# Performance work log

Measured on AMD Instinct MI355X. Metric: run time of the kernel, lower is better.

Reference implementation:

```python
import jax, jax.numpy as jnp
import numpy as np

B, T, C = 4, 2048, 1024
H = 16
D = C // H  # head_dim = 64


def setup_inputs() -> dict:
    key = jax.random.key(0)
    k1, k2, k3 = jax.random.split(key, 3)
    scale = 0.02
    x = jax.random.normal(k1, (B, T, C), dtype=jnp.float32)
    w_attn = jax.random.normal(k2, (C, 3 * C), dtype=jnp.float32) * scale
    b_attn = jnp.zeros((3 * C,), dtype=jnp.float32)
    w_proj = jax.random.normal(k3, (C, C), dtype=jnp.float32) * scale
    b_proj = jnp.zeros((C,), dtype=jnp.float32)
    return {"x": x, "w_attn": w_attn, "b_attn": b_attn,
            "w_proj": w_proj, "b_proj": b_proj}


def reference(x, w_attn, b_attn, w_proj, b_proj):
    Bc, Tc, Cc = x.shape
    qkv = x @ w_attn + b_attn                      # [B, T, 3C]
    q, k, v = jnp.split(qkv, 3, axis=-1)
    # [B, H, T, D]
    q = q.reshape(Bc, Tc, H, D).transpose(0, 2, 1, 3)
    k = k.reshape(Bc, Tc, H, D).transpose(0, 2, 1, 3)
    v = v.reshape(Bc, Tc, H, D).transpose(0, 2, 1, 3)
    att = jnp.einsum('bhqd,bhkd->bhqk', q, k) / jnp.sqrt(jnp.float32(D))
    causal = jnp.tril(jnp.ones((Tc, Tc), dtype=bool))
    att = jnp.where(causal, att, -jnp.inf)
    att = jax.nn.softmax(att, axis=-1)
    y = jnp.einsum('bhqk,bhkd->bhqd', att, v)      # [B, H, T, D]
    y = y.transpose(0, 2, 1, 3).reshape(Bc, Tc, Cc)
    return y @ w_proj + b_proj
```

## Files before the change

kernel.cpp:

```cpp
#include <hip/hip_runtime.h>

typedef unsigned short u16;
typedef __bf16 bf16x8 __attribute__((ext_vector_type(8)));
typedef float f32x4 __attribute__((ext_vector_type(4)));

#define T_SEQ 2048
#define NH 16
#define HD 64
#define CDIM 1024

__device__ __forceinline__ u16 f2bf(float f) {
    union { float f; unsigned int u; } v; v.f = f;
    unsigned int r = v.u + 0x7FFFu + ((v.u >> 16) & 1u);
    return (u16)(r >> 16);
}

__device__ __forceinline__ unsigned cvt_pk_bf16(float lo, float hi) {
    unsigned r;
    asm("v_cvt_pk_bf16_f32 %0, %1, %2" : "=v"(r) : "v"(lo), "v"(hi));
    return r;
}

__device__ __forceinline__ void gll16(const u16* g, const u16* l) {
    __builtin_amdgcn_global_load_lds((const __attribute__((address_space(1))) void*)g,
                                     (__attribute__((address_space(3))) void*)l, 16, 0, 0);
}

__global__ void cast_f32_bf16(const float* __restrict__ in, u16* __restrict__ out, int n) {
    int i = (blockIdx.x * blockDim.x + threadIdx.x) * 4;
    if (i >= n) return;
    float4 v = *reinterpret_cast<const float4*>(in + i);
    ushort4 o;
    o.x = f2bf(v.x); o.y = f2bf(v.y); o.z = f2bf(v.z); o.w = f2bf(v.w);
    *reinterpret_cast<ushort4*>(out + i) = o;
}

__global__ void transpose_cast(const float* __restrict__ in, u16* __restrict__ out, int K, int N) {
    __shared__ float tile[32][33];
    int n0 = blockIdx.x * 32, k0 = blockIdx.y * 32;
    int tx = threadIdx.x & 31, ty = threadIdx.x >> 5;
#pragma unroll
    for (int i = 0; i < 32; i += 8)
        tile[ty + i][tx] = in[(size_t)(k0 + ty + i) * N + n0 + tx];
    __syncthreads();
#pragma unroll
    for (int i = 0; i < 32; i += 8)
        out[(size_t)(n0 + ty + i) * K + k0 + tx] = f2bf(tile[tx][ty + i]);
}

__global__ void vtrans(const u16* __restrict__ in, u16* __restrict__ out) {
    __shared__ u16 tl[32][34];
    int x0 = blockIdx.x * 32;
    int y0 = blockIdx.y * 32;
    int z = blockIdx.z;
    int tx = threadIdx.x & 31, ty = threadIdx.x >> 5;
    const size_t ib = (size_t)z * T_SEQ * HD;
    const size_t ob = (size_t)z * HD * T_SEQ;
#pragma unroll
    for (int i = 0; i < 32; i += 8)
        tl[ty + i][tx] = in[ib + (size_t)(x0 + ty + i) * HD + y0 + tx];
    __syncthreads();
#pragma unroll
    for (int i = 0; i < 32; i += 8)
        out[ob + (size_t)(y0 + ty + i) * T_SEQ + x0 + tx] = tl[tx][ty + i];
}

template <int EPI>
__global__ __launch_bounds__(256)
void gemm_bt(const u16* __restrict__ A, const u16* __restrict__ Bt,
             const float* __restrict__ bias, float* __restrict__ out,
             u16* __restrict__ qb, u16* __restrict__ kb, u16* __restrict__ vb,
             int M, int N, int K) {
    __shared__ u16 As[128 * 64];
    __shared__ u16 Bs[128 * 64];
    const int tid = threadIdx.x;
    const int lane = tid & 63;
    const int w = tid >> 6;
    const int wm = w >> 1, wn = w & 1;
    const int c = lane & 15, g = lane >> 4;
    const int gm0 = blockIdx.y * 128;
    const int gn0 = blockIdx.x * 128;

    f32x4 acc[4][4] = {};

    for (int k0 = 0; k0 < K; k0 += 64) {
#pragma unroll
        for (int it = 0; it < 4; ++it) {
            int tb = it * 256 + w * 64;
            int task = tb + lane;
            int r = task >> 3, sl = task & 7;
            int sc = sl ^ (r & 7);
            gll16(A + (size_t)(gm0 + r) * K + k0 + sc * 8, As + (size_t)task * 8);
            gll16(Bt + (size_t)(gn0 + r) * K + k0 + sc * 8, Bs + (size_t)task * 8);
        }
        __syncthreads();
#pragma unroll
        for (int kk = 0; kk < 2; ++kk) {
            bf16x8 a[4], b[4];
#pragma unroll
            for (int m = 0; m < 4; ++m) {
                int row = wm * 64 + m * 16 + c;
                a[m] = *reinterpret_cast<const bf16x8*>(&As[row * 64 + (((kk * 4 + g) ^ (c & 7)) * 8)]);
            }
#pragma unroll
            for (int n = 0; n < 4; ++n) {
                int row = wn * 64 + n * 16 + c;
                b[n] = *reinterpret_cast<const bf16x8*>(&Bs[row * 64 + (((kk * 4 + g) ^ (c & 7)) * 8)]);
            }
#pragma unroll
            for (int m = 0; m < 4; ++m)
#pragma unroll
                for (int n = 0; n < 4; ++n)
                    acc[m][n] = __builtin_amdgcn_mfma_f32_16x16x32_bf16(a[m], b[n], acc[m][n], 0, 0, 0);
        }
        __syncthreads();
    }

#pragma unroll
    for (int m = 0; m < 4; ++m) {
#pragma unroll
        for (int n = 0; n < 4; ++n) {
            int gcol = gn0 + wn * 64 + n * 16 + c;
            float bv = bias[gcol];
#pragma unroll
            for (int r = 0; r < 4; ++r) {
                int grow = gm0 + wm * 64 + m * 16 + g * 4 + r;
                float v = acc[m][n][r] + bv;
                if (EPI == 1) {
                    out[(size_t)grow * N + gcol] = v;
                } else {
                    int which = gcol >> 10;
                    int cc = gcol & 1023;
                    int h = cc >> 6, d = cc & 63;
                    int b_ = grow >> 11, t = grow & 2047;
                    int bh = b_ * NH + h;
                    u16 bvv = (which == 0) ? f2bf(v * 0.18033688f) : f2bf(v);
                    u16* dst = (which == 0) ? qb : (which == 1) ? kb : vb;
                    dst[((size_t)bh * T_SEQ + t) * HD + d] = bvv;
                }
            }
        }
    }
}

__global__ __launch_bounds__(512, 4)
void attn_fwd(const u16* __restrict__ Qb, const u16* __restrict__ Kb,
              const u16* __restrict__ Vt, u16* __restrict__ yb) {
    __shared__ u16 Ks[2][64 * 64];
    __shared__ u16 Vs[2][64 * 64];
    __shared__ unsigned Ps[8][1024];
    const int tid = threadIdx.x, lane = tid & 63, w = tid >> 6;
    const int g = lane >> 4, c = lane & 15;
    const int f = blockIdx.x;
    const int xcd = f & 7, j = (f >> 3) & 7, bhi = f >> 6;
    const int bh = xcd * 8 + bhi;
    const int b = bh >> 4, hh = bh & 15;
    const float NEG = -1e30f;
    const size_t kBase = (size_t)bh * T_SEQ * HD;
    const size_t vBase = (size_t)bh * HD * T_SEQ;
    unsigned* ps = &Ps[w][0];
    const int sw = c & 7;
    const int qwv[2] = {(15 - j) * 128 + w * 16, j * 128 + w * 16};

    bf16x8 qf[2][2];
#pragma unroll
    for (int u = 0; u < 2; ++u) {
        const u16* qrow = Qb + kBase + (size_t)(qwv[u] + c) * HD;
        qf[u][0] = *reinterpret_cast<const bf16x8*>(qrow + g * 8);
        qf[u][1] = *reinterpret_cast<const bf16x8*>(qrow + 32 + g * 8);
    }

    f32x4 yacc[2][4] = {};
    float l[2] = {0.f, 0.f};
    const int nt = 2 * (15 - j) + 2;
    int cur = 0;

    {
        int r = tid >> 3, sl = tid & 7, sc = sl ^ (r & 7);
        gll16(Kb + kBase + (size_t)r * HD + sc * 8, Ks[0] + (size_t)tid * 8);
        gll16(Vt + vBase + (size_t)r * T_SEQ + sc * 8, Vs[0] + (size_t)tid * 8);
        __syncthreads();
    }

    for (int kt = 0; kt < nt; ++kt) {
        const int kv0 = kt * 64;
        const bool more = (kt + 1 < nt);
        if (more) {
            const int nv0 = kv0 + 64;
            int r = tid >> 3, sl = tid & 7, sc = sl ^ (r & 7);
            gll16(Kb + kBase + (size_t)(nv0 + r) * HD + sc * 8, Ks[cur ^ 1] + (size_t)tid * 8);
            gll16(Vt + vBase + (size_t)r * T_SEQ + nv0 + sc * 8, Vs[cur ^ 1] + (size_t)tid * 8);
        }
        const u16* ks = Ks[cur];
        const u16* vs = Vs[cur];
        const bool a0 = (kv0 <= qwv[0] + 15);
        const bool a1 = (kv0 <= qwv[1] + 15);

        if (a0 || a1) {
            f32x4 s_[2][4];
            __builtin_amdgcn_s_setprio(1);
#pragma unroll
            for (int n = 0; n < 4; ++n) {
                int rb = (n * 16 + c) * 64;
                bf16x8 k0 = *reinterpret_cast<const bf16x8*>(&ks[rb + ((g ^ sw) * 8)]);
                bf16x8 k1 = *reinterpret_cast<const bf16x8*>(&ks[rb + (((4 + g) ^ sw) * 8)]);
                if (a0) {
                    f32x4 t = {};
                    t = __builtin_amdgcn_mfma_f32_16x16x32_bf16(k0, qf[0][0], t, 0, 0, 0);
                    t = __builtin_amdgcn_mfma_f32_16x16x32_bf16(k1, qf[0][1], t, 0, 0, 0);
                    s_[0][n] = t;
                }
                if (a1) {
                    f32x4 t = {};
                    t = __builtin_amdgcn_mfma_f32_16x16x32_bf16(k0, qf[1][0], t, 0, 0, 0);
                    t = __builtin_amdgcn_mfma_f32_16x16x32_bf16(k1, qf[1][1], t, 0, 0, 0);
                    s_[1][n] = t;
                }
            }
            __builtin_amdgcn_s_setprio(0);

            bf16x8 pa[2][2];
#pragma unroll
            for (int u = 0; u < 2; ++u) {
                const bool act = u ? a1 : a0;
                if (act) {
                    const int qwu = qwv[u];
                    if (kv0 + 63 > qwu) {
                        int q = qwu + c;
#pragma unroll
                        for (int n = 0; n < 4; ++n) {
                            int kvb = kv0 + n * 16 + 4 * g;
#pragma unroll
                            for (int r = 0; r < 4; ++r)
                                if (kvb + r > q) s_[u][n][r] = NEG;
                        }
                    }
                    float rsum = 0.f;
                    int base = (16 * u + c) * 32;
#pragma unroll
                    for (int n = 0; n < 4; ++n) {
                        float p0 = __builtin_amdgcn_exp2f(s_[u][n][0]);
                        float p1 = __builtin_amdgcn_exp2f(s_[u][n][1]);
                        float p2 = __builtin_amdgcn_exp2f(s_[u][n][2]);
                        float p3 = __builtin_amdgcn_exp2f(s_[u][n][3]);
                        rsum += (p0 + p1) + (p2 + p3);
                        uint2 pr;
                        pr.x = cvt_pk_bf16(p0, p1);
                        pr.y = cvt_pk_bf16(p2, p3);
                        *reinterpret_cast<uint2*>(&ps[base + ((n ^ (c & 3)) << 3) + 2 * g]) = pr;
                    }
                    l[u] += rsum;
#pragma unroll
                    for (int kk = 0; kk < 2; ++kk) {
                        int idx = (16 * u + c) * 32 + ((kk * 16 + 4 * g) ^ ((c & 3) << 3));
                        pa[u][kk] = *reinterpret_cast<const bf16x8*>(&ps[idx]);
                    }
                }
            }
            __builtin_amdgcn_s_setprio(1);
#pragma unroll
            for (int n = 0; n < 4; ++n) {
                int rb = (n * 16 + c) * 64;
                bf16x8 v0 = *reinterpret_cast<const bf16x8*>(&vs[rb + ((g ^ sw) * 8)]);
                bf16x8 v1 = *reinterpret_cast<const bf16x8*>(&vs[rb + (((4 + g) ^ sw) * 8)]);
                if (a0) {
                    yacc[0][n] = __builtin_amdgcn_mfma_f32_16x16x32_bf16(pa[0][0], v0, yacc[0][n], 0, 0, 0);
                    yacc[0][n] = __builtin_amdgcn_mfma_f32_16x16x32_bf16(pa[0][1], v1, yacc[0][n], 0, 0, 0);
                }
                if (a1) {
                    yacc[1][n] = __builtin_amdgcn_mfma_f32_16x16x32_bf16(pa[1][0], v0, yacc[1][n], 0, 0, 0);
                    yacc[1][n] = __builtin_amdgcn_mfma_f32_16x16x32_bf16(pa[1][1], v1, yacc[1][n], 0, 0, 0);
                }
            }
            __builtin_amdgcn_s_setprio(0);
        }
        if (more) __syncthreads();
        cur ^= 1;
    }
#pragma unroll
    for (int u = 0; u < 2; ++u) {
        float lt = l[u];
        lt += __shfl_xor(lt, 16);
        lt += __shfl_xor(lt, 32);
        float linv = 1.f / lt;
        float lr[4];
#pragma unroll
        for (int r = 0; r < 4; ++r) lr[r] = __shfl(linv, g * 4 + r);
#pragma unroll
        for (int r = 0; r < 4; ++r) {
            int q = qwv[u] + g * 4 + r;
#pragma unroll
            for (int n = 0; n < 4; ++n)
                yb[((size_t)b * T_SEQ + q) * CDIM + hh * HD + n * 16 + c] = f2bf(yacc[u][n][r] * lr[r]);
        }
    }
}

extern "C" void kernel_launch(void* const* d_in, const int* in_sizes, int n_in,
                              void* d_out, int out_size, void* d_ws, size_t ws_size,
                              hipStream_t stream) {
    const float* x      = (const float*)d_in[0];
    const float* w_attn = (const float*)d_in[1];
    const float* b_attn = (const float*)d_in[2];
    const float* w_proj = (const float*)d_in[3];
    const float* b_proj = (const float*)d_in[4];
    float* out = (float*)d_out;

    u16* ws  = (u16*)d_ws;
    u16* xb  = ws;
    u16* wT  = xb  + (size_t)8192 * 1024;
    u16* wpT = wT  + (size_t)3072 * 1024;
    u16* Qb  = wpT + (size_t)1024 * 1024;
    u16* Kb  = Qb  + (size_t)64 * 2048 * 64;
    u16* Vt  = Kb  + (size_t)64 * 2048 * 64;
    u16* yb  = Vt  + (size_t)64 * 2048 * 64;
    u16* vb  = yb;

    cast_f32_bf16<<<8192, 256, 0, stream>>>(x, xb, 8192 * 1024);
    transpose_cast<<<dim3(96, 32), 256, 0, stream>>>(w_attn, wT, 1024, 3072);
    transpose_cast<<<dim3(32, 32), 256, 0, stream>>>(w_proj, wpT, 1024, 1024);
    gemm_bt<0><<<dim3(24, 64), 256, 0, stream>>>(xb, wT, b_attn, nullptr, Qb, Kb, vb,
                                                 8192, 3072, 1024);
    vtrans<<<dim3(64, 2, 64), 256, 0, stream>>>(vb, Vt);
    attn_fwd<<<512, 512, 0, stream>>>(Qb, Kb, Vt, yb);
    gemm_bt<1><<<dim3(8, 64), 256, 0, stream>>>(yb, wpT, b_proj, out, nullptr, nullptr, nullptr,
                                                8192, 1024, 1024);
}
```

Baseline: 181.9 us.

## Triple-buffer GEMM loads with 256x128 tiles and a single barrier per k-step

The shared GEMM kernel moves from a single-buffered 128x128x64 tile with two barriers per iteration to a 256x128 tile with a K-step of 32, triple-buffered in LDS. Direct global-to-LDS loads for the next two stages are issued ahead, and vmcnt waits let the loads overlap the MFMA work. It also raises wave priority around the MFMA block and doubles the per-wave accumulator count. The goal is to hide load latency and improve data reuse. The cost is higher register pressure and fewer blocks: the projection GEMM drops to 256 blocks, which may underfill the GPU's compute units.

```diff
diff --git a/kernel.cpp b/kernel.cpp
--- a/kernel.cpp
+++ b/kernel.cpp
@@ -66,66 +66,86 @@
 }
 
 template <int EPI>
-__global__ __launch_bounds__(256)
+__global__ __launch_bounds__(256, 2)
 void gemm_bt(const u16* __restrict__ A, const u16* __restrict__ Bt,
              const float* __restrict__ bias, float* __restrict__ out,
              u16* __restrict__ qb, u16* __restrict__ kb, u16* __restrict__ vb,
              int M, int N, int K) {
-    __shared__ u16 As[128 * 64];
-    __shared__ u16 Bs[128 * 64];
+    __shared__ u16 As[3][256 * 32];
+    __shared__ u16 Bs[3][128 * 32];
     const int tid = threadIdx.x;
     const int lane = tid & 63;
     const int w = tid >> 6;
     const int wm = w >> 1, wn = w & 1;
     const int c = lane & 15, g = lane >> 4;
-    const int gm0 = blockIdx.y * 128;
+    const int gm0 = blockIdx.y * 256;
     const int gn0 = blockIdx.x * 128;
-
-    f32x4 acc[4][4] = {};
-
-    for (int k0 = 0; k0 < K; k0 += 64) {
+    const int NT = K >> 5;
+
+    f32x4 acc[8][4] = {};
+
+    auto STAGE = [&](int t, int buf) {
+        const int k0 = t << 5;
 #pragma unroll
         for (int it = 0; it < 4; ++it) {
-            int tb = it * 256 + w * 64;
-            int task = tb + lane;
-            int r = task >> 3, sl = task & 7;
-            int sc = sl ^ (r & 7);
-            gll16(A + (size_t)(gm0 + r) * K + k0 + sc * 8, As + (size_t)task * 8);
-            gll16(Bt + (size_t)(gn0 + r) * K + k0 + sc * 8, Bs + (size_t)task * 8);
-        }
-        __syncthreads();
-#pragma unroll
-        for (int kk = 0; kk < 2; ++kk) {
-            bf16x8 a[4], b[4];
-#pragma unroll
-            for (int m = 0; m < 4; ++m) {
-                int row = wm * 64 + m * 16 + c;
-                a[m] = *reinterpret_cast<const bf16x8*>(&As[row * 64 + (((kk * 4 + g) ^ (c & 7)) * 8)]);
-            }
-#pragma unroll
-            for (int n = 0; n < 4; ++n) {
-                int row = wn * 64 + n * 16 + c;
-                b[n] = *reinterpret_cast<const bf16x8*>(&Bs[row * 64 + (((kk * 4 + g) ^ (c & 7)) * 8)]);
-            }
-#pragma unroll
-            for (int m = 0; m < 4; ++m)
-#pragma unroll
-                for (int n = 0; n < 4; ++n)
-                    acc[m][n] = __builtin_amdgcn_mfma_f32_16x16x32_bf16(a[m], b[n], acc[m][n], 0, 0, 0);
-        }
-        __syncthreads();
-    }
-
-#pragma unroll
-    for (int m = 0; m < 4; ++m) {
+            int task = tid + it * 256;
+            int r = task >> 2, sl = task & 3, sc = sl ^ (r & 3);
+            gll16(A + (size_t)(gm0 + r) * K + k0 + sc * 8, As[buf] + (size_t)task * 8);
+        }
+#pragma unroll
+        for (int it = 0; it < 2; ++it) {
+            int task = tid + it * 256;
+            int r = task >> 2, sl = task & 3, sc = sl ^ (r & 3);
+            gll16(Bt + (size_t)(gn0 + r) * K + k0 + sc * 8, Bs[buf] + (size_t)task * 8);
+        }
+    };
+
+    STAGE(0, 0);
+    STAGE(1, 1);
+    asm volatile("s_waitcnt vmcnt(6)" ::: "memory");
+    __builtin_amdgcn_s_barrier();
+    asm volatile("" ::: "memory");
+
+    for (int t = 0; t < NT; ++t) {
+        if (t + 2 < NT) STAGE(t + 2, (t + 2) % 3);
+        const u16* as = As[t % 3];
+        const u16* bs = Bs[t % 3];
+        bf16x8 a[8], b[4];
+#pragma unroll
+        for (int mi = 0; mi < 8; ++mi) {
+            int row = wm * 128 + mi * 16 + c;
+            a[mi] = *reinterpret_cast<const bf16x8*>(&as[row * 32 + ((g ^ (c & 3)) * 8)]);
+        }
 #pragma unroll
         for (int n = 0; n < 4; ++n) {
-            int gcol = gn0 + wn * 64 + n * 16 + c;
-            float bv = bias[gcol];
+            int row = wn * 64 + n * 16 + c;
+            b[n] = *reinterpret_cast<const bf16x8*>(&bs[row * 32 + ((g ^ (c & 3)) * 8)]);
+        }
+        __builtin_amdgcn_s_setprio(1);
+#pragma unroll
+        for (int mi = 0; mi < 8; ++mi)
+#pragma unroll
+            for (int n = 0; n < 4; ++n)
+                acc[mi][n] = __builtin_amdgcn_mfma_f32_16x16x32_bf16(a[mi], b[n], acc[mi][n], 0, 0, 0);
+        __builtin_amdgcn_s_setprio(0);
+        if (t + 1 < NT) {
+            if (t + 2 < NT) asm volatile("s_waitcnt vmcnt(6)" ::: "memory");
+            else            asm volatile("s_waitcnt vmcnt(0)" ::: "memory");
+            __builtin_amdgcn_s_barrier();
+            asm volatile("" ::: "memory");
+        }
+    }
+
+#pragma unroll
+    for (int n = 0; n < 4; ++n) {
+        int gcol = gn0 + wn * 64 + n * 16 + c;
+        float bv = bias[gcol];
+#pragma unroll
+        for (int mi = 0; mi < 8; ++mi) {
 #pragma unroll
             for (int r = 0; r < 4; ++r) {
-                int grow = gm0 + wm * 64 + m * 16 + g * 4 + r;
-                float v = acc[m][n][r] + bv;
+                int grow = gm0 + wm * 128 + mi * 16 + g * 4 + r;
+                float v = acc[mi][n][r] + bv;
                 if (EPI == 1) {
                     out[(size_t)grow * N + gcol] = v;
                 } else {
@@ -319,10 +339,10 @@
     cast_f32_bf16<<<8192, 256, 0, stream>>>(x, xb, 8192 * 1024);
     transpose_cast<<<dim3(96, 32), 256, 0, stream>>>(w_attn, wT, 1024, 3072);
     transpose_cast<<<dim3(32, 32), 256, 0, stream>>>(w_proj, wpT, 1024, 1024);
-    gemm_bt<0><<<dim3(24, 64), 256, 0, stream>>>(xb, wT, b_attn, nullptr, Qb, Kb, vb,
+    gemm_bt<0><<<dim3(24, 32), 256, 0, stream>>>(xb, wT, b_attn, nullptr, Qb, Kb, vb,
                                                  8192, 3072, 1024);
     vtrans<<<dim3(64, 2, 64), 256, 0, stream>>>(vb, Vt);
     attn_fwd<<<512, 512, 0, stream>>>(Qb, Kb, Vt, yb);
-    gemm_bt<1><<<dim3(8, 64), 256, 0, stream>>>(yb, wpT, b_proj, out, nullptr, nullptr, nullptr,
+    gemm_bt<1><<<dim3(8, 32), 256, 0, stream>>>(yb, wpT, b_proj, out, nullptr, nullptr, nullptr,
                                                 8192, 1024, 1024);
 }
```

New measurement: 214.7 us. 1.18x slower.
